# Kernel tuning notes

Measured on AMD Instinct MI355X. Metric: run time of the kernel, lower is better.

## Reference

```python
import jax, jax.numpy as jnp
import numpy as np

EPS = 1e-12      # F.normalize eps
LN_EPS = 1e-5    # nn.LayerNorm eps
SLOPE = 0.01     # LeakyReLU negative slope
SCALE = 5.0      # attention temperature used by the module


def _l2norm(x):
    n = jnp.sqrt(jnp.sum(x * x, axis=-1, keepdims=True))
    return x / jnp.maximum(n, EPS)


def _layer_norm(x, g, b):
    m = jnp.mean(x, axis=-1, keepdims=True)
    v = jnp.mean((x - m) ** 2, axis=-1, keepdims=True)
    return (x - m) / jnp.sqrt(v + LN_EPS) * g + b


def _leaky(x):
    return jnp.where(x >= 0, x, SLOPE * x)


def setup_inputs() -> dict:
    key = jax.random.key(0)
    ks = jax.random.split(key, 18)
    B, T, N, C = 8, 8, 25, 256
    n = T * N  # 200 == num_nodes
    inp = {
        "local_feat": jax.random.normal(ks[0], (B, T, N, C), dtype=jnp.float32),
        "global_feat": jax.random.normal(ks[1], (B, C), dtype=jnp.float32),
        "pos": jax.random.uniform(ks[2], (B, T, N, 9), dtype=jnp.float32),
        # Diff_prop params
        "dp_adj_w": jax.random.normal(ks[3], (C, C), dtype=jnp.float32) / np.sqrt(C),
        "dp_aff_w": jax.random.normal(ks[4], (C, C), dtype=jnp.float32) * np.sqrt(2.0 / C),
        "dp_aff_b": jnp.zeros((C,), dtype=jnp.float32),
        "dp_ln_g": jnp.ones((C,), dtype=jnp.float32),
        "dp_ln_b": jnp.zeros((C,), dtype=jnp.float32),
        # Feat_aggr params
        "fa_adj_w": jax.random.normal(ks[5], (C, C), dtype=jnp.float32) / np.sqrt(C),
        "fa_aff_w": jax.random.normal(ks[6], (C, C), dtype=jnp.float32) * np.sqrt(2.0 / C),
        "fa_aff_b": jnp.zeros((C,), dtype=jnp.float32),
        "fa_ln_g": jnp.ones((C,), dtype=jnp.float32),
        "fa_ln_b": jnp.zeros((C,), dtype=jnp.float32),
        # Node_att params (Linear(num_nodes+9, 1): weight [1, n+9])
        "na_w": jax.random.normal(ks[7], (1, n + 9), dtype=jnp.float32) * np.sqrt(2.0 / (n + 9)),
        "na_b": jnp.zeros((1,), dtype=jnp.float32),
    }
    return inp


def _diff_prop(lf4, adj_w, aff_w, aff_b, ln_g, ln_b):
    B, T, N, C = lf4.shape
    n = T * N
    lf = lf4.reshape(B, n, C)
    nf = _l2norm(lf)
    # quadratic-form attention: A[b,i,j] = nf_i W nf_j
    A = jnp.einsum('bnc,cd,bmd->bnm', nf, adj_w, nf)
    A = jnp.exp(SCALE * (A - jnp.max(A, axis=-1, keepdims=True)))
    A = A * (1.0 - jnp.eye(n, dtype=A.dtype))
    A = A / jnp.maximum(jnp.sum(A, axis=-1, keepdims=True), EPS)  # L1 row norm (A>=0)
    # full pairwise difference tensor [B, n, n, C]
    diff = lf[:, :, None, :] - lf[:, None, :, :]
    diff = jnp.einsum('bijc,dc->bijd', diff, aff_w) + aff_b
    agg = jnp.einsum('bij,bijd->bid', A, diff)
    out = _leaky(_layer_norm(agg, ln_g, ln_b))
    return out.reshape(B, T, N, C)


def _feat_aggr(lf4, adj_w, aff_w, aff_b, ln_g, ln_b):
    B, T, N, C = lf4.shape
    n = T * N
    lf = lf4.reshape(B, n, C)
    nf = _l2norm(lf)
    A = jnp.einsum('bnc,cd,bmd->bnm', nf, adj_w, nf)
    A = jax.nn.softmax(SCALE * (A - jnp.max(A, axis=-1, keepdims=True)), axis=-1)
    lf = jnp.einsum('bnc,dc->bnd', lf, aff_w) + aff_b
    lf = jnp.einsum('bij,bjk->bik', A, lf)
    out = _leaky(_layer_norm(lf, ln_g, ln_b))
    return out.reshape(B, T, N, C)


def _node_att(lf4, pos, w, b):
    B, T, N, C = lf4.shape
    n = T * N
    lf = lf4.reshape(B, n, C)
    p = pos.reshape(B, n, -1)
    nf = _l2norm(lf)
    A = jnp.einsum('bnc,bmc->bnm', nf, nf)            # [B, n, n]
    src = jnp.concatenate([A, p], axis=-1)            # [B, n, n+9]
    att = jax.nn.sigmoid(jnp.einsum('bni,oi->bno', src, w) + b)  # [B, n, 1]
    att = att.reshape(B, T, N, 1)
    return lf4 * att


def reference(local_feat, global_feat, pos,
              dp_adj_w, dp_aff_w, dp_aff_b, dp_ln_g, dp_ln_b,
              fa_adj_w, fa_aff_w, fa_aff_b, fa_ln_g, fa_ln_b,
              na_w, na_b):
    x = _diff_prop(local_feat, dp_adj_w, dp_aff_w, dp_aff_b, dp_ln_g, dp_ln_b)
    x = _feat_aggr(x, fa_adj_w, fa_aff_w, fa_aff_b, fa_ln_g, fa_ln_b)
    x = _node_att(x, pos, na_w, na_b)
    return x
```

## Files before the change

### kernel.cpp

```cpp
#include <hip/hip_runtime.h>
#include <math.h>

#define Bn 8
#define NN 200
#define Cc 256
#define RR (Bn*NN)
#define JP 200
#define N_EPS 1e-12f
#define LN_EPS 1e-5f
#define SLOPE 0.01f
#define SCALE 5.0f

#define FMA4(acc, s, v) { acc.x = fmaf((s), (v).x, acc.x); acc.y = fmaf((s), (v).y, acc.y); \
                          acc.z = fmaf((s), (v).z, acc.z); acc.w = fmaf((s), (v).w, acc.w); }

__device__ __forceinline__ float wave_reduce_sum(float v) {
    #pragma unroll
    for (int o = 32; o > 0; o >>= 1) v += __shfl_xor(v, o);
    return v;
}

__device__ __forceinline__ float2 half_reduce_sum2(float2 v, float* sh, int h) {
    __syncthreads();
    #pragma unroll
    for (int o = 32; o > 0; o >>= 1) { v.x += __shfl_xor(v.x, o); v.y += __shfl_xor(v.y, o); }
    int w = threadIdx.x >> 6;
    if ((threadIdx.x & 63) == 0) { sh[w*2] = v.x; sh[w*2+1] = v.y; }
    __syncthreads();
    int b0 = h * 8;
    return make_float2(sh[b0]+sh[b0+2]+sh[b0+4]+sh[b0+6],
                       sh[b0+1]+sh[b0+3]+sh[b0+5]+sh[b0+7]);
}

__device__ __forceinline__ float2 half_reduce_max2(float2 v, float* sh, int h) {
    __syncthreads();
    #pragma unroll
    for (int o = 32; o > 0; o >>= 1) {
        v.x = fmaxf(v.x, __shfl_xor(v.x, o));
        v.y = fmaxf(v.y, __shfl_xor(v.y, o));
    }
    int w = threadIdx.x >> 6;
    if ((threadIdx.x & 63) == 0) { sh[w*2] = v.x; sh[w*2+1] = v.y; }
    __syncthreads();
    int b0 = h * 8;
    return make_float2(fmaxf(fmaxf(sh[b0],sh[b0+2]), fmaxf(sh[b0+4],sh[b0+6])),
                       fmaxf(fmaxf(sh[b0+1],sh[b0+3]), fmaxf(sh[b0+5],sh[b0+7])));
}

__global__ void k_pre(const float* __restrict__ lf, const float* __restrict__ dp_adj_w,
                      const float* __restrict__ dp_aff_w, const float* __restrict__ fa_aff_w,
                      float* __restrict__ nfT, float* __restrict__ M,
                      float* __restrict__ WT1, float* __restrict__ WT2) {
    __shared__ __align__(16) float sx[8][Cc];
    __shared__ __align__(16) float buf[8192];
    __shared__ float tile[32][33];
    int bid = blockIdx.x;
    int t = threadIdx.x, lane = t & 63, wvi = t >> 6;
    if (bid < RR/8) {
        int r0 = bid * 8;
        #pragma unroll
        for (int k = 0; k < 2; k++) {
            int r = 2*wvi + k;
            float4 x = ((const float4*)(lf + (size_t)(r0 + r) * Cc))[lane];
            float ss = wave_reduce_sum(x.x*x.x + x.y*x.y + x.z*x.z + x.w*x.w);
            float inv = 1.f / fmaxf(sqrtf(ss), N_EPS);
            x.x *= inv; x.y *= inv; x.z *= inv; x.w *= inv;
            ((float4*)&sx[r][0])[lane] = x;
        }
        __syncthreads();
        {
            int b = r0 / NN, i0 = r0 % NN;
            float4 cA, cB;
            cA.x = sx[0][t]; cA.y = sx[1][t]; cA.z = sx[2][t]; cA.w = sx[3][t];
            cB.x = sx[4][t]; cB.y = sx[5][t]; cB.z = sx[6][t]; cB.w = sx[7][t];
            float* np = nfT + (size_t)b * Cc * JP + (size_t)t * JP + i0;
            *((float4*)np) = cA;
            *((float4*)(np + 4)) = cB;
        }
        int qc = t & 63, cid = t >> 6;
        int c0 = cid * 64;
        float4 z = make_float4(0.f,0.f,0.f,0.f);
        float4 acc0=z, acc1=z, acc2=z, acc3=z, acc4=z, acc5=z, acc6=z, acc7=z;
        #pragma unroll 4
        for (int c4 = c0; c4 < c0 + 64; c4 += 4) {
            float4 w0 = *(const float4*)(dp_adj_w + (size_t)(c4+0) * Cc + 4*qc);
            float4 w1 = *(const float4*)(dp_adj_w + (size_t)(c4+1) * Cc + 4*qc);
            float4 w2 = *(const float4*)(dp_adj_w + (size_t)(c4+2) * Cc + 4*qc);
            float4 w3 = *(const float4*)(dp_adj_w + (size_t)(c4+3) * Cc + 4*qc);
            float4 xr;
            xr = *(const float4*)(&sx[0][c4]);
            FMA4(acc0, xr.x, w0); FMA4(acc0, xr.y, w1); FMA4(acc0, xr.z, w2); FMA4(acc0, xr.w, w3);
            xr = *(const float4*)(&sx[1][c4]);
            FMA4(acc1, xr.x, w0); FMA4(acc1, xr.y, w1); FMA4(acc1, xr.z, w2); FMA4(acc1, xr.w, w3);
            xr = *(const float4*)(&sx[2][c4]);
            FMA4(acc2, xr.x, w0); FMA4(acc2, xr.y, w1); FMA4(acc2, xr.z, w2); FMA4(acc2, xr.w, w3);
            xr = *(const float4*)(&sx[3][c4]);
            FMA4(acc3, xr.x, w0); FMA4(acc3, xr.y, w1); FMA4(acc3, xr.z, w2); FMA4(acc3, xr.w, w3);
            xr = *(const float4*)(&sx[4][c4]);
            FMA4(acc4, xr.x, w0); FMA4(acc4, xr.y, w1); FMA4(acc4, xr.z, w2); FMA4(acc4, xr.w, w3);
            xr = *(const float4*)(&sx[5][c4]);
            FMA4(acc5, xr.x, w0); FMA4(acc5, xr.y, w1); FMA4(acc5, xr.z, w2); FMA4(acc5, xr.w, w3);
            xr = *(const float4*)(&sx[6][c4]);
            FMA4(acc6, xr.x, w0); FMA4(acc6, xr.y, w1); FMA4(acc6, xr.z, w2); FMA4(acc6, xr.w, w3);
            xr = *(const float4*)(&sx[7][c4]);
            FMA4(acc7, xr.x, w0); FMA4(acc7, xr.y, w1); FMA4(acc7, xr.z, w2); FMA4(acc7, xr.w, w3);
        }
        float4* b4 = (float4*)buf;
        int o = cid * 512 + qc;
        b4[o      ] = acc0; b4[o +  64] = acc1; b4[o + 128] = acc2; b4[o + 192] = acc3;
        b4[o + 256] = acc4; b4[o + 320] = acc5; b4[o + 384] = acc6; b4[o + 448] = acc7;
        __syncthreads();
        #pragma unroll
        for (int k = 0; k < 2; k++) {
            int o4 = t + k*256;
            int r = o4 >> 6, qc2 = o4 & 63;
            float4 s0 = b4[o4], s1 = b4[512 + o4], s2 = b4[1024 + o4], s3 = b4[1536 + o4];
            float4 sv;
            sv.x = (s0.x + s1.x) + (s2.x + s3.x);
            sv.y = (s0.y + s1.y) + (s2.y + s3.y);
            sv.z = (s0.z + s1.z) + (s2.z + s3.z);
            sv.w = (s0.w + s1.w) + (s2.w + s3.w);
            *(float4*)(M + (size_t)(r0 + r) * Cc + 4*qc2) = sv;
        }
    } else {
        int tb = bid - RR/8;
        const float* S; float* D;
        if (tb < 64) { S = dp_aff_w; D = WT1; } else { S = fa_aff_w; D = WT2; tb -= 64; }
        int bx = tb & 7, by = tb >> 3;
        int tx = t & 31, ty = t >> 5;
        #pragma unroll
        for (int k = 0; k < 32; k += 8)
            tile[ty + k][tx] = S[(size_t)(by*32 + ty + k) * Cc + bx*32 + tx];
        __syncthreads();
        #pragma unroll
        for (int k = 0; k < 32; k += 8)
            D[(size_t)(bx*32 + ty + k) * Cc + by*32 + tx] = tile[tx][ty + k];
    }
}

__global__ void k_row1f(const float* __restrict__ nfT, const float* __restrict__ Min,
                        const float* __restrict__ lf, const float* __restrict__ dp_aff_b,
                        const float* __restrict__ WT1,
                        const float* __restrict__ g, const float* __restrict__ bb,
                        const float* __restrict__ fa_adj_w, const float* __restrict__ WT2,
                        const float* __restrict__ fa_aff_b,
                        float* __restrict__ nfT2, float* __restrict__ M2,
                        float* __restrict__ lf2) {
    __shared__ __align__(16) float smT[Cc*4];
    __shared__ __align__(16) float saraw[4*NN];
    __shared__ __align__(16) float saT[NN*4];
    __shared__ __align__(16) float suT[Cc*4];
    __shared__ __align__(16) float buf[8192];
    __shared__ float sh[16];
    __shared__ float sinv[4];
    int t = threadIdx.x, h = t >> 8, tt = t & 255;
    int b = blockIdx.x & 7;
    int i0 = (blockIdx.x >> 3) * 4;
    size_t base = (size_t)b * NN * Cc;
    {
        const float* src = Min + base + (size_t)i0 * Cc;
        #pragma unroll
        for (int o = t; o < 1024; o += 512) {
            int c = o >> 2, r = o & 3;
            smT[o] = src[(size_t)r * Cc + c];
        }
    }
    __syncthreads();
    {
        int q = t & 63, cid = t >> 6;
        if (q < 50) {
            int c0 = cid * 32;
            const float* nfp = nfT + (size_t)b * Cc * JP + (size_t)c0 * JP + 4*q;
            float4 z4 = make_float4(0.f,0.f,0.f,0.f);
            float4 a0 = z4, a1 = z4, a2 = z4, a3 = z4;
            #pragma unroll 8
            for (int c = 0; c < 32; c++) {
                float4 v  = *(const float4*)(nfp + (size_t)c * JP);
                float4 mv = *(const float4*)(&smT[(c0 + c) * 4]);
                FMA4(a0, mv.x, v); FMA4(a1, mv.y, v);
                FMA4(a2, mv.z, v); FMA4(a3, mv.w, v);
            }
            float* pp = buf + cid * 800 + 4*q;
            *(float4*)(pp      ) = a0;
            *(float4*)(pp + 200) = a1;
            *(float4*)(pp + 400) = a2;
            *(float4*)(pp + 600) = a3;
        }
    }
    __syncthreads();
    for (int o = t; o < 800; o += 512) {
        float s = 0.f;
        #pragma unroll
        for (int p = 0; p < 8; p++) s += buf[p*800 + o];
        saraw[o] = s;
    }
    __syncthreads();
    int lr0 = h, lr1 = h + 2;
    float2 vm;
    vm.x = (tt < NN) ? saraw[lr0*NN + tt] : -INFINITY;
    vm.y = (tt < NN) ? saraw[lr1*NN + tt] : -INFINITY;
    float2 m = half_reduce_max2(vm, sh, h);
    float e0 = (tt < NN && tt != i0 + lr0) ? expf(SCALE * (vm.x - m.x)) : 0.f;
    float e1 = (tt < NN && tt != i0 + lr1) ? expf(SCALE * (vm.y - m.y)) : 0.f;
    float2 sum = half_reduce_sum2(make_float2(e0, e1), sh, h);
    if (tt < NN) {
        saT[tt*4 + lr0] = e0 / fmaxf(sum.x, N_EPS);
        saT[tt*4 + lr1] = e1 / fmaxf(sum.y, N_EPS);
    }
    float s0 = sum.x / fmaxf(sum.x, N_EPS);
    float s1 = sum.y / fmaxf(sum.y, N_EPS);
    __syncthreads();
    const float* lfb = lf + base;
    {
        int qc = t & 63, jc = t >> 6;
        int j0 = jc * 25;
        float4 z4 = make_float4(0.f,0.f,0.f,0.f);
        float4 u0 = z4, u1 = z4, u2 = z4, u3 = z4;
        #pragma unroll 5
        for (int j = j0; j < j0 + 25; j++) {
            float4 pv = *(const float4*)(lfb + (size_t)j * Cc + 4*qc);
            float4 av = *(const float4*)(&saT[j*4]);
            FMA4(u0, av.x, pv); FMA4(u1, av.y, pv);
            FMA4(u2, av.z, pv); FMA4(u3, av.w, pv);
        }
        float* pp = buf + jc*1024 + 4*qc;
        *(float4*)(pp      ) = u0;
        *(float4*)(pp + 256) = u1;
        *(float4*)(pp + 512) = u2;
        *(float4*)(pp + 768) = u3;
    }
    __syncthreads();
    float acc0 = 0.f, acc1 = 0.f;
    #pragma unroll
    for (int p = 0; p < 8; p++) { acc0 += buf[p*1024 + t]; acc1 += buf[p*1024 + t + 512]; }
    float U0 = fmaf(s0, lfb[(size_t)(i0 + lr0) * Cc + tt], -acc0);
    float U1 = fmaf(s1, lfb[(size_t)(i0 + lr1) * Cc + tt], -acc1);
    __syncthreads();
    smT[tt*4 + lr0] = U0;
    smT[tt*4 + lr1] = U1;
    __syncthreads();
    {
        int qc = t & 63, cid = t >> 6;
        int c0 = cid * 32;
        float4 z4 = make_float4(0.f,0.f,0.f,0.f);
        float4 p0 = z4, p1 = z4, p2 = z4, p3 = z4;
        #pragma unroll 8
        for (int c = c0; c < c0 + 32; c++) {
            float4 wv = *(const float4*)(WT1 + (size_t)c * Cc + 4*qc);
            float4 uv = *(const float4*)(&smT[c*4]);
            FMA4(p0, uv.x, wv); FMA4(p1, uv.y, wv);
            FMA4(p2, uv.z, wv); FMA4(p3, uv.w, wv);
        }
        float* pp = buf + cid*1024 + 4*qc;
        *(float4*)(pp      ) = p0;
        *(float4*)(pp + 256) = p1;
        *(float4*)(pp + 512) = p2;
        *(float4*)(pp + 768) = p3;
    }
    __syncthreads();
    float y0 = 0.f, y1 = 0.f;
    #pragma unroll
    for (int p = 0; p < 8; p++) { y0 += buf[p*1024 + t]; y1 += buf[p*1024 + t + 512]; }
    float bv = dp_aff_b[tt];
    y0 += s0 * bv;
    y1 += s1 * bv;
    float gg = g[tt], bbv = bb[tt];
    float2 mean2 = half_reduce_sum2(make_float2(y0, y1), sh, h);
    float d0 = y0 - mean2.x * (1.f/256.f);
    float d1 = y1 - mean2.y * (1.f/256.f);
    float2 var2 = half_reduce_sum2(make_float2(d0*d0, d1*d1), sh, h);
    float z0 = d0 / sqrtf(var2.x * (1.f/256.f) + LN_EPS) * gg + bbv;
    float z1 = d1 / sqrtf(var2.y * (1.f/256.f) + LN_EPS) * gg + bbv;
    z0 = (z0 >= 0.f) ? z0 : SLOPE * z0;
    z1 = (z1 >= 0.f) ? z1 : SLOPE * z1;
    suT[tt*4 + lr0] = z0; suT[tt*4 + lr1] = z1;
    float2 ss2 = half_reduce_sum2(make_float2(z0*z0, z1*z1), sh, h);
    if (tt == 0) {
        sinv[lr0] = 1.f / fmaxf(sqrtf(ss2.x), N_EPS);
        sinv[lr1] = 1.f / fmaxf(sqrtf(ss2.y), N_EPS);
    }
    __syncthreads();
    if (h == 0) {
        float4 col;
        col.x = suT[tt*4+0] * sinv[0]; col.y = suT[tt*4+1] * sinv[1];
        col.z = suT[tt*4+2] * sinv[2]; col.w = suT[tt*4+3] * sinv[3];
        *((float4*)(nfT2 + (size_t)b * Cc * JP + (size_t)tt * JP + i0)) = col;
    }
    {
        int qc = t & 63, gidx = t >> 6;
        int mt = gidx & 1, cch = gidx >> 1;
        const float* Wm = mt ? WT2 : fa_adj_w;
        int c0 = cch * 64;
        float4 z4 = make_float4(0.f,0.f,0.f,0.f);
        float4 d0v = z4, d1v = z4, d2v = z4, d3v = z4;
        #pragma unroll 8
        for (int c = c0; c < c0 + 64; c++) {
            float4 wv = *(const float4*)(Wm + (size_t)c * Cc + 4*qc);
            float4 uv = *(const float4*)(&suT[c*4]);
            FMA4(d0v, uv.x, wv); FMA4(d1v, uv.y, wv);
            FMA4(d2v, uv.z, wv); FMA4(d3v, uv.w, wv);
        }
        float* pp = buf + cch*2048 + mt*1024 + 4*qc;
        *(float4*)(pp      ) = d0v;
        *(float4*)(pp + 256) = d1v;
        *(float4*)(pp + 512) = d2v;
        *(float4*)(pp + 768) = d3v;
    }
    __syncthreads();
    {
        float4* b4 = (float4*)buf;
        int o4 = t;
        int mt2 = o4 >> 8, r2 = (o4 >> 6) & 3, qc2 = o4 & 63;
        float4 v0 = b4[o4], v1 = b4[512 + o4], v2 = b4[1024 + o4], v3 = b4[1536 + o4];
        float4 sv;
        sv.x = (v0.x + v1.x) + (v2.x + v3.x);
        sv.y = (v0.y + v1.y) + (v2.y + v3.y);
        sv.z = (v0.z + v1.z) + (v2.z + v3.z);
        sv.w = (v0.w + v1.w) + (v2.w + v3.w);
        if (mt2 == 0) {
            float sc = sinv[r2];
            sv.x *= sc; sv.y *= sc; sv.z *= sc; sv.w *= sc;
            *(float4*)(M2 + base + (size_t)(i0 + r2) * Cc + 4*qc2) = sv;
        } else {
            float4 fb = *(const float4*)(fa_aff_b + 4*qc2);
            sv.x += fb.x; sv.y += fb.y; sv.z += fb.z; sv.w += fb.w;
            *(float4*)(lf2 + base + (size_t)(i0 + r2) * Cc + 4*qc2) = sv;
        }
    }
}

__global__ void k_row2f(const float* __restrict__ nfT2, const float* __restrict__ M2,
                        const float* __restrict__ lf2, const float* __restrict__ g,
                        const float* __restrict__ bb, float* __restrict__ x2,
                        float* __restrict__ nf3) {
    __shared__ __align__(16) float smT[Cc*4];
    __shared__ __align__(16) float saraw[4*NN];
    __shared__ __align__(16) float saT[NN*4];
    __shared__ __align__(16) float buf[8192];
    __shared__ float sh[16];
    int t = threadIdx.x, h = t >> 8, tt = t & 255;
    int b = blockIdx.x & 7;
    int i0 = (blockIdx.x >> 3) * 4;
    size_t base = (size_t)b * NN * Cc;
    {
        const float* src = M2 + base + (size_t)i0 * Cc;
        #pragma unroll
        for (int o = t; o < 1024; o += 512) {
            int c = o >> 2, r = o & 3;
            smT[o] = src[(size_t)r * Cc + c];
        }
    }
    __syncthreads();
    {
        int q = t & 63, cid = t >> 6;
        if (q < 50) {
            int c0 = cid * 32;
            const float* nfp = nfT2 + (size_t)b * Cc * JP + (size_t)c0 * JP + 4*q;
            float4 z4 = make_float4(0.f,0.f,0.f,0.f);
            float4 a0 = z4, a1 = z4, a2 = z4, a3 = z4;
            #pragma unroll 8
            for (int c = 0; c < 32; c++) {
                float4 v  = *(const float4*)(nfp + (size_t)c * JP);
                float4 mv = *(const float4*)(&smT[(c0 + c) * 4]);
                FMA4(a0, mv.x, v); FMA4(a1, mv.y, v);
                FMA4(a2, mv.z, v); FMA4(a3, mv.w, v);
            }
            float* pp = buf + cid * 800 + 4*q;
            *(float4*)(pp      ) = a0;
            *(float4*)(pp + 200) = a1;
            *(float4*)(pp + 400) = a2;
            *(float4*)(pp + 600) = a3;
        }
    }
    __syncthreads();
    for (int o = t; o < 800; o += 512) {
        float s = 0.f;
        #pragma unroll
        for (int p = 0; p < 8; p++) s += buf[p*800 + o];
        saraw[o] = s;
    }
    __syncthreads();
    int lr0 = h, lr1 = h + 2;
    float2 vm;
    vm.x = (tt < NN) ? saraw[lr0*NN + tt] : -INFINITY;
    vm.y = (tt < NN) ? saraw[lr1*NN + tt] : -INFINITY;
    float2 m = half_reduce_max2(vm, sh, h);
    float e0 = (tt < NN) ? expf(SCALE * (vm.x - m.x)) : 0.f;
    float e1 = (tt < NN) ? expf(SCALE * (vm.y - m.y)) : 0.f;
    float2 sum = half_reduce_sum2(make_float2(e0, e1), sh, h);
    if (tt < NN) { saT[tt*4 + lr0] = e0 / sum.x; saT[tt*4 + lr1] = e1 / sum.y; }
    __syncthreads();
    const float* l2b = lf2 + base;
    {
        int qc = t & 63, jc = t >> 6;
        int j0 = jc * 25;
        float4 z4 = make_float4(0.f,0.f,0.f,0.f);
        float4 u0 = z4, u1 = z4, u2 = z4, u3 = z4;
        #pragma unroll 5
        for (int j = j0; j < j0 + 25; j++) {
            float4 pv = *(const float4*)(l2b + (size_t)j * Cc + 4*qc);
            float4 av = *(const float4*)(&saT[j*4]);
            FMA4(u0, av.x, pv); FMA4(u1, av.y, pv);
            FMA4(u2, av.z, pv); FMA4(u3, av.w, pv);
        }
        float* pp = buf + jc*1024 + 4*qc;
        *(float4*)(pp      ) = u0;
        *(float4*)(pp + 256) = u1;
        *(float4*)(pp + 512) = u2;
        *(float4*)(pp + 768) = u3;
    }
    __syncthreads();
    float y0 = 0.f, y1 = 0.f;
    #pragma unroll
    for (int p = 0; p < 8; p++) { y0 += buf[p*1024 + t]; y1 += buf[p*1024 + t + 512]; }
    float gg = g[tt], bbv = bb[tt];
    float2 mean2 = half_reduce_sum2(make_float2(y0, y1), sh, h);
    float d0 = y0 - mean2.x * (1.f/256.f);
    float d1 = y1 - mean2.y * (1.f/256.f);
    float2 var2 = half_reduce_sum2(make_float2(d0*d0, d1*d1), sh, h);
    float z0 = d0 / sqrtf(var2.x * (1.f/256.f) + LN_EPS) * gg + bbv;
    float z1 = d1 / sqrtf(var2.y * (1.f/256.f) + LN_EPS) * gg + bbv;
    z0 = (z0 >= 0.f) ? z0 : SLOPE * z0;
    z1 = (z1 >= 0.f) ? z1 : SLOPE * z1;
    x2[base + (size_t)(i0 + lr0) * Cc + tt] = z0;
    x2[base + (size_t)(i0 + lr1) * Cc + tt] = z1;
    float2 ss2 = half_reduce_sum2(make_float2(z0*z0, z1*z1), sh, h);
    nf3[base + (size_t)(i0 + lr0) * Cc + tt] = z0 / fmaxf(sqrtf(ss2.x), N_EPS);
    nf3[base + (size_t)(i0 + lr1) * Cc + tt] = z1 / fmaxf(sqrtf(ss2.y), N_EPS);
}

__global__ void k_natt(const float* __restrict__ x2, const float* __restrict__ nf3,
                       const float* __restrict__ pos, const float* __restrict__ w,
                       const float* __restrict__ nb, float* __restrict__ out) {
    __shared__ float svb[4][Cc];
    int t = threadIdx.x, lane = t & 63, wv = t >> 6;
    int b = blockIdx.x & 7;
    int i = (blockIdx.x >> 3) * 4 + wv;
    const float4* slab = (const float4*)(nf3 + (size_t)b * NN * Cc);
    float4 acc = make_float4(0.f, 0.f, 0.f, 0.f);
    for (int j = wv * 50; j < wv * 50 + 50; j++) {
        float4 q = slab[j * 64 + lane];
        float wj = w[j];
        acc.x = fmaf(wj, q.x, acc.x);
        acc.y = fmaf(wj, q.y, acc.y);
        acc.z = fmaf(wj, q.z, acc.z);
        acc.w = fmaf(wj, q.w, acc.w);
    }
    ((float4*)&svb[wv][0])[lane] = acc;
    __syncthreads();
    float4 p0 = ((const float4*)&svb[0][0])[lane];
    float4 p1 = ((const float4*)&svb[1][0])[lane];
    float4 p2 = ((const float4*)&svb[2][0])[lane];
    float4 p3 = ((const float4*)&svb[3][0])[lane];
    float4 vb;
    vb.x = (p0.x + p1.x) + (p2.x + p3.x);
    vb.y = (p0.y + p1.y) + (p2.y + p3.y);
    vb.z = (p0.z + p1.z) + (p2.z + p3.z);
    vb.w = (p0.w + p1.w) + (p2.w + p3.w);
    size_t bi = (size_t)b * NN + i;
    float4 nv = ((const float4*)(nf3 + bi * Cc))[lane];
    float val = nv.x*vb.x + nv.y*vb.y + nv.z*vb.z + nv.w*vb.w;
    if (lane < 9) val += pos[bi * 9 + lane] * w[NN + lane];
    val = wave_reduce_sum(val);
    float att = 1.f / (1.f + expf(-(val + nb[0])));
    float4 xo = ((const float4*)(x2 + bi * Cc))[lane];
    xo.x *= att; xo.y *= att; xo.z *= att; xo.w *= att;
    ((float4*)(out + bi * Cc))[lane] = xo;
}

extern "C" void kernel_launch(void* const* d_in, const int* in_sizes, int n_in,
                              void* d_out, int out_size, void* d_ws, size_t ws_size,
                              hipStream_t stream) {
    (void)in_sizes; (void)n_in; (void)out_size; (void)ws_size;
    const float* lf       = (const float*)d_in[0];
    const float* pos      = (const float*)d_in[2];
    const float* dp_adj_w = (const float*)d_in[3];
    const float* dp_aff_w = (const float*)d_in[4];
    const float* dp_aff_b = (const float*)d_in[5];
    const float* dp_ln_g  = (const float*)d_in[6];
    const float* dp_ln_b  = (const float*)d_in[7];
    const float* fa_adj_w = (const float*)d_in[8];
    const float* fa_aff_w = (const float*)d_in[9];
    const float* fa_aff_b = (const float*)d_in[10];
    const float* fa_ln_g  = (const float*)d_in[11];
    const float* fa_ln_b  = (const float*)d_in[12];
    const float* na_w     = (const float*)d_in[13];
    const float* na_b     = (const float*)d_in[14];
    float* out = (float*)d_out;
    float* ws  = (float*)d_ws;

    float* nfT  = ws;
    float* nfT2 = nfT  + Bn * Cc * JP;
    float* M    = nfT2 + Bn * Cc * JP;
    float* lf2  = M    + RR * Cc;
    float* x2   = lf2  + RR * Cc;
    float* nf3  = x2   + RR * Cc;
    float* WT1  = nf3  + RR * Cc;
    float* WT2  = WT1  + Cc * Cc;

    k_pre  <<<RR/8 + 128, dim3(256), 0, stream>>>(lf, dp_adj_w, dp_aff_w, fa_aff_w,
                                                  nfT, M, WT1, WT2);
    k_row1f<<<Bn * NN/4,  dim3(512), 0, stream>>>(nfT, M, lf, dp_aff_b, WT1,
                                                  dp_ln_g, dp_ln_b, fa_adj_w, WT2, fa_aff_b,
                                                  nfT2, M, lf2);
    k_row2f<<<Bn * NN/4,  dim3(512), 0, stream>>>(nfT2, M, lf2, fa_ln_g, fa_ln_b, x2, nf3);
    k_natt <<<Bn * NN/4,  dim3(256), 0, stream>>>(x2, nf3, pos, na_w, na_b, out);
}
```

Before: 61.73 us.

## Process eight rows per block in k_row1f to reuse weight loads

k_row1f now handles 8 query rows per block instead of 4, halving the grid. The weight GEMM phases (WT1, fa_adj_w, WT2) each load a weight float4 once and apply it to 8 rows, halving global weight traffic per row. In exchange the block count drops to 200, which reduces parallelism on a large GPU. Shared memory use and per-thread register pressure also grow, and the attention phases run twice serially.

```diff
diff --git a/kernel.cpp b/kernel.cpp
--- a/kernel.cpp
+++ b/kernel.cpp
@@ -146,186 +146,226 @@
                         const float* __restrict__ fa_aff_b,
                         float* __restrict__ nfT2, float* __restrict__ M2,
                         float* __restrict__ lf2) {
-    __shared__ __align__(16) float smT[Cc*4];
-    __shared__ __align__(16) float saraw[4*NN];
-    __shared__ __align__(16) float saT[NN*4];
-    __shared__ __align__(16) float suT[Cc*4];
+    __shared__ __align__(16) float smT[Cc*8];
+    __shared__ __align__(16) float saraw[8*NN];
+    __shared__ __align__(16) float saT[NN*8];
+    __shared__ __align__(16) float suT[Cc*8];
     __shared__ __align__(16) float buf[8192];
     __shared__ float sh[16];
-    __shared__ float sinv[4];
+    __shared__ float sinv[8];
     int t = threadIdx.x, h = t >> 8, tt = t & 255;
     int b = blockIdx.x & 7;
-    int i0 = (blockIdx.x >> 3) * 4;
+    int i0 = (blockIdx.x >> 3) * 8;
     size_t base = (size_t)b * NN * Cc;
     {
         const float* src = Min + base + (size_t)i0 * Cc;
         #pragma unroll
-        for (int o = t; o < 1024; o += 512) {
-            int c = o >> 2, r = o & 3;
+        for (int o = t; o < 2048; o += 512) {
+            int c = o >> 3, r = o & 7;
             smT[o] = src[(size_t)r * Cc + c];
         }
     }
     __syncthreads();
-    {
-        int q = t & 63, cid = t >> 6;
-        if (q < 50) {
-            int c0 = cid * 32;
-            const float* nfp = nfT + (size_t)b * Cc * JP + (size_t)c0 * JP + 4*q;
+    #pragma unroll
+    for (int p = 0; p < 2; p++) {
+        {
+            int q = t & 63, cid = t >> 6;
+            if (q < 50) {
+                int c0 = cid * 32;
+                const float* nfp = nfT + (size_t)b * Cc * JP + (size_t)c0 * JP + 4*q;
+                float4 z4 = make_float4(0.f,0.f,0.f,0.f);
+                float4 a0 = z4, a1 = z4, a2 = z4, a3 = z4;
+                #pragma unroll 8
+                for (int c = 0; c < 32; c++) {
+                    float4 v  = *(const float4*)(nfp + (size_t)c * JP);
+                    float4 mv = *(const float4*)(&smT[(c0 + c) * 8 + 4*p]);
+                    FMA4(a0, mv.x, v); FMA4(a1, mv.y, v);
+                    FMA4(a2, mv.z, v); FMA4(a3, mv.w, v);
+                }
+                float* pp = buf + cid * 800 + 4*q;
+                *(float4*)(pp      ) = a0;
+                *(float4*)(pp + 200) = a1;
+                *(float4*)(pp + 400) = a2;
+                *(float4*)(pp + 600) = a3;
+            }
+        }
+        __syncthreads();
+        for (int o = t; o < 800; o += 512) {
+            float s = 0.f;
+            #pragma unroll
+            for (int q8 = 0; q8 < 8; q8++) s += buf[q8*800 + o];
+            saraw[p*800 + o] = s;
+        }
+        __syncthreads();
+    }
+    float sv[4];
+    #pragma unroll
+    for (int k = 0; k < 2; k++) {
+        int rA = 4*k + h, rB = 4*k + h + 2;
+        float2 vm;
+        vm.x = (tt < NN) ? saraw[rA*NN + tt] : -INFINITY;
+        vm.y = (tt < NN) ? saraw[rB*NN + tt] : -INFINITY;
+        float2 m = half_reduce_max2(vm, sh, h);
+        float e0 = (tt < NN && tt != i0 + rA) ? expf(SCALE * (vm.x - m.x)) : 0.f;
+        float e1 = (tt < NN && tt != i0 + rB) ? expf(SCALE * (vm.y - m.y)) : 0.f;
+        float2 sum = half_reduce_sum2(make_float2(e0, e1), sh, h);
+        if (tt < NN) {
+            saT[tt*8 + rA] = e0 / fmaxf(sum.x, N_EPS);
+            saT[tt*8 + rB] = e1 / fmaxf(sum.y, N_EPS);
+        }
+        sv[2*k]   = sum.x / fmaxf(sum.x, N_EPS);
+        sv[2*k+1] = sum.y / fmaxf(sum.y, N_EPS);
+    }
+    __syncthreads();
+    const float* lfb = lf + base;
+    #pragma unroll
+    for (int p = 0; p < 2; p++) {
+        {
+            int qc = t & 63, jc = t >> 6;
+            int j0 = jc * 25;
             float4 z4 = make_float4(0.f,0.f,0.f,0.f);
-            float4 a0 = z4, a1 = z4, a2 = z4, a3 = z4;
-            #pragma unroll 8
-            for (int c = 0; c < 32; c++) {
-                float4 v  = *(const float4*)(nfp + (size_t)c * JP);
-                float4 mv = *(const float4*)(&smT[(c0 + c) * 4]);
-                FMA4(a0, mv.x, v); FMA4(a1, mv.y, v);
-                FMA4(a2, mv.z, v); FMA4(a3, mv.w, v);
+            float4 u0 = z4, u1 = z4, u2 = z4, u3 = z4;
+            #pragma unroll 5
+            for (int j = j0; j < j0 + 25; j++) {
+                float4 pv = *(const float4*)(lfb + (size_t)j * Cc + 4*qc);
+                float4 av = *(const float4*)(&saT[j*8 + 4*p]);
+                FMA4(u0, av.x, pv); FMA4(u1, av.y, pv);
+                FMA4(u2, av.z, pv); FMA4(u3, av.w, pv);
             }
-            float* pp = buf + cid * 800 + 4*q;
-            *(float4*)(pp      ) = a0;
-            *(float4*)(pp + 200) = a1;
-            *(float4*)(pp + 400) = a2;
-            *(float4*)(pp + 600) = a3;
-        }
-    }
-    __syncthreads();
-    for (int o = t; o < 800; o += 512) {
-        float s = 0.f;
-        #pragma unroll
-        for (int p = 0; p < 8; p++) s += buf[p*800 + o];
-        saraw[o] = s;
-    }
-    __syncthreads();
-    int lr0 = h, lr1 = h + 2;
-    float2 vm;
-    vm.x = (tt < NN) ? saraw[lr0*NN + tt] : -INFINITY;
-    vm.y = (tt < NN) ? saraw[lr1*NN + tt] : -INFINITY;
-    float2 m = half_reduce_max2(vm, sh, h);
-    float e0 = (tt < NN && tt != i0 + lr0) ? expf(SCALE * (vm.x - m.x)) : 0.f;
-    float e1 = (tt < NN && tt != i0 + lr1) ? expf(SCALE * (vm.y - m.y)) : 0.f;
-    float2 sum = half_reduce_sum2(make_float2(e0, e1), sh, h);
-    if (tt < NN) {
-        saT[tt*4 + lr0] = e0 / fmaxf(sum.x, N_EPS);
-        saT[tt*4 + lr1] = e1 / fmaxf(sum.y, N_EPS);
-    }
-    float s0 = sum.x / fmaxf(sum.x, N_EPS);
-    float s1 = sum.y / fmaxf(sum.y, N_EPS);
-    __syncthreads();
-    const float* lfb = lf + base;
-    {
-        int qc = t & 63, jc = t >> 6;
-        int j0 = jc * 25;
-        float4 z4 = make_float4(0.f,0.f,0.f,0.f);
-        float4 u0 = z4, u1 = z4, u2 = z4, u3 = z4;
-        #pragma unroll 5
-        for (int j = j0; j < j0 + 25; j++) {
-            float4 pv = *(const float4*)(lfb + (size_t)j * Cc + 4*qc);
-            float4 av = *(const float4*)(&saT[j*4]);
-            FMA4(u0, av.x, pv); FMA4(u1, av.y, pv);
-            FMA4(u2, av.z, pv); FMA4(u3, av.w, pv);
-        }
-        float* pp = buf + jc*1024 + 4*qc;
-        *(float4*)(pp      ) = u0;
-        *(float4*)(pp + 256) = u1;
-        *(float4*)(pp + 512) = u2;
-        *(float4*)(pp + 768) = u3;
-    }
-    __syncthreads();
-    float acc0 = 0.f, acc1 = 0.f;
-    #pragma unroll
-    for (int p = 0; p < 8; p++) { acc0 += buf[p*1024 + t]; acc1 += buf[p*1024 + t + 512]; }
-    float U0 = fmaf(s0, lfb[(size_t)(i0 + lr0) * Cc + tt], -acc0);
-    float U1 = fmaf(s1, lfb[(size_t)(i0 + lr1) * Cc + tt], -acc1);
-    __syncthreads();
-    smT[tt*4 + lr0] = U0;
-    smT[tt*4 + lr1] = U1;
-    __syncthreads();
+            float* pp = buf + jc*1024 + 4*qc;
+            *(float4*)(pp      ) = u0;
+            *(float4*)(pp + 256) = u1;
+            *(float4*)(pp + 512) = u2;
+            *(float4*)(pp + 768) = u3;
+        }
+        __syncthreads();
+        float acc0 = 0.f, acc1 = 0.f;
+        #pragma unroll
+        for (int q8 = 0; q8 < 8; q8++) { acc0 += buf[q8*1024 + t]; acc1 += buf[q8*1024 + t + 512]; }
+        int rA = 4*p + h, rB = 4*p + h + 2;
+        float U0 = fmaf(sv[2*p],   lfb[(size_t)(i0 + rA) * Cc + tt], -acc0);
+        float U1 = fmaf(sv[2*p+1], lfb[(size_t)(i0 + rB) * Cc + tt], -acc1);
+        smT[tt*8 + rA] = U0;
+        smT[tt*8 + rB] = U1;
+        __syncthreads();
+    }
     {
         int qc = t & 63, cid = t >> 6;
-        int c0 = cid * 32;
-        float4 z4 = make_float4(0.f,0.f,0.f,0.f);
-        float4 p0 = z4, p1 = z4, p2 = z4, p3 = z4;
-        #pragma unroll 8
-        for (int c = c0; c < c0 + 32; c++) {
-            float4 wv = *(const float4*)(WT1 + (size_t)c * Cc + 4*qc);
-            float4 uv = *(const float4*)(&smT[c*4]);
-            FMA4(p0, uv.x, wv); FMA4(p1, uv.y, wv);
-            FMA4(p2, uv.z, wv); FMA4(p3, uv.w, wv);
-        }
-        float* pp = buf + cid*1024 + 4*qc;
-        *(float4*)(pp      ) = p0;
-        *(float4*)(pp + 256) = p1;
-        *(float4*)(pp + 512) = p2;
-        *(float4*)(pp + 768) = p3;
-    }
-    __syncthreads();
-    float y0 = 0.f, y1 = 0.f;
-    #pragma unroll
-    for (int p = 0; p < 8; p++) { y0 += buf[p*1024 + t]; y1 += buf[p*1024 + t + 512]; }
-    float bv = dp_aff_b[tt];
-    y0 += s0 * bv;
-    y1 += s1 * bv;
+        if (cid < 4) {
+            int c0 = cid * 64;
+            float4 z4 = make_float4(0.f,0.f,0.f,0.f);
+            float4 pA0=z4,pA1=z4,pA2=z4,pA3=z4,pB0=z4,pB1=z4,pB2=z4,pB3=z4;
+            #pragma unroll 4
+            for (int c = c0; c < c0 + 64; c++) {
+                float4 wv = *(const float4*)(WT1 + (size_t)c * Cc + 4*qc);
+                float4 uA = *(const float4*)(&smT[c*8]);
+                float4 uB = *(const float4*)(&smT[c*8 + 4]);
+                FMA4(pA0, uA.x, wv); FMA4(pA1, uA.y, wv);
+                FMA4(pA2, uA.z, wv); FMA4(pA3, uA.w, wv);
+                FMA4(pB0, uB.x, wv); FMA4(pB1, uB.y, wv);
+                FMA4(pB2, uB.z, wv); FMA4(pB3, uB.w, wv);
+            }
+            float* pp = buf + cid*2048 + 4*qc;
+            *(float4*)(pp       ) = pA0; *(float4*)(pp +  256) = pA1;
+            *(float4*)(pp +  512) = pA2; *(float4*)(pp +  768) = pA3;
+            *(float4*)(pp + 1024) = pB0; *(float4*)(pp + 1280) = pB1;
+            *(float4*)(pp + 1536) = pB2; *(float4*)(pp + 1792) = pB3;
+        }
+    }
+    __syncthreads();
+    float y0, y1, y2, y3;
+    {
+        float bv = dp_aff_b[tt];
+        int rA = h, rB = h + 2, rC = 4 + h, rD = 6 + h;
+        y0 = sv[0]*bv; y1 = sv[1]*bv; y2 = sv[2]*bv; y3 = sv[3]*bv;
+        #pragma unroll
+        for (int q8 = 0; q8 < 4; q8++) {
+            y0 += buf[q8*2048 + rA*256 + tt];
+            y1 += buf[q8*2048 + rB*256 + tt];
+            y2 += buf[q8*2048 + rC*256 + tt];
+            y3 += buf[q8*2048 + rD*256 + tt];
+        }
+    }
     float gg = g[tt], bbv = bb[tt];
-    float2 mean2 = half_reduce_sum2(make_float2(y0, y1), sh, h);
-    float d0 = y0 - mean2.x * (1.f/256.f);
-    float d1 = y1 - mean2.y * (1.f/256.f);
-    float2 var2 = half_reduce_sum2(make_float2(d0*d0, d1*d1), sh, h);
-    float z0 = d0 / sqrtf(var2.x * (1.f/256.f) + LN_EPS) * gg + bbv;
-    float z1 = d1 / sqrtf(var2.y * (1.f/256.f) + LN_EPS) * gg + bbv;
-    z0 = (z0 >= 0.f) ? z0 : SLOPE * z0;
-    z1 = (z1 >= 0.f) ? z1 : SLOPE * z1;
-    suT[tt*4 + lr0] = z0; suT[tt*4 + lr1] = z1;
-    float2 ss2 = half_reduce_sum2(make_float2(z0*z0, z1*z1), sh, h);
-    if (tt == 0) {
-        sinv[lr0] = 1.f / fmaxf(sqrtf(ss2.x), N_EPS);
-        sinv[lr1] = 1.f / fmaxf(sqrtf(ss2.y), N_EPS);
+    #pragma unroll
+    for (int k = 0; k < 2; k++) {
+        float ya = (k == 0) ? y0 : y2;
+        float yb = (k == 0) ? y1 : y3;
+        int rA = 4*k + h, rB = 4*k + h + 2;
+        float2 mean2 = half_reduce_sum2(make_float2(ya, yb), sh, h);
+        float d0 = ya - mean2.x * (1.f/256.f);
+        float d1 = yb - mean2.y * (1.f/256.f);
+        float2 var2 = half_reduce_sum2(make_float2(d0*d0, d1*d1), sh, h);
+        float z0 = d0 / sqrtf(var2.x * (1.f/256.f) + LN_EPS) * gg + bbv;
+        float z1 = d1 / sqrtf(var2.y * (1.f/256.f) + LN_EPS) * gg + bbv;
+        z0 = (z0 >= 0.f) ? z0 : SLOPE * z0;
+        z1 = (z1 >= 0.f) ? z1 : SLOPE * z1;
+        suT[tt*8 + rA] = z0;
+        suT[tt*8 + rB] = z1;
+        float2 ss2 = half_reduce_sum2(make_float2(z0*z0, z1*z1), sh, h);
+        if (tt == 0) {
+            sinv[rA] = 1.f / fmaxf(sqrtf(ss2.x), N_EPS);
+            sinv[rB] = 1.f / fmaxf(sqrtf(ss2.y), N_EPS);
+        }
     }
     __syncthreads();
     if (h == 0) {
-        float4 col;
-        col.x = suT[tt*4+0] * sinv[0]; col.y = suT[tt*4+1] * sinv[1];
-        col.z = suT[tt*4+2] * sinv[2]; col.w = suT[tt*4+3] * sinv[3];
-        *((float4*)(nfT2 + (size_t)b * Cc * JP + (size_t)tt * JP + i0)) = col;
-    }
-    {
-        int qc = t & 63, gidx = t >> 6;
-        int mt = gidx & 1, cch = gidx >> 1;
+        float4 cA, cB;
+        cA.x = suT[tt*8+0]*sinv[0]; cA.y = suT[tt*8+1]*sinv[1];
+        cA.z = suT[tt*8+2]*sinv[2]; cA.w = suT[tt*8+3]*sinv[3];
+        cB.x = suT[tt*8+4]*sinv[4]; cB.y = suT[tt*8+5]*sinv[5];
+        cB.z = suT[tt*8+6]*sinv[6]; cB.w = suT[tt*8+7]*sinv[7];
+        float* np = nfT2 + (size_t)b * Cc * JP + (size_t)tt * JP + i0;
+        *((float4*)np) = cA;
+        *((float4*)(np + 4)) = cB;
+    }
+    #pragma unroll
+    for (int mt = 0; mt < 2; mt++) {
         const float* Wm = mt ? WT2 : fa_adj_w;
-        int c0 = cch * 64;
-        float4 z4 = make_float4(0.f,0.f,0.f,0.f);
-        float4 d0v = z4, d1v = z4, d2v = z4, d3v = z4;
-        #pragma unroll 8
-        for (int c = c0; c < c0 + 64; c++) {
-            float4 wv = *(const float4*)(Wm + (size_t)c * Cc + 4*qc);
-            float4 uv = *(const float4*)(&suT[c*4]);
-            FMA4(d0v, uv.x, wv); FMA4(d1v, uv.y, wv);
-            FMA4(d2v, uv.z, wv); FMA4(d3v, uv.w, wv);
-        }
-        float* pp = buf + cch*2048 + mt*1024 + 4*qc;
-        *(float4*)(pp      ) = d0v;
-        *(float4*)(pp + 256) = d1v;
-        *(float4*)(pp + 512) = d2v;
-        *(float4*)(pp + 768) = d3v;
-    }
-    __syncthreads();
-    {
-        float4* b4 = (float4*)buf;
-        int o4 = t;
-        int mt2 = o4 >> 8, r2 = (o4 >> 6) & 3, qc2 = o4 & 63;
-        float4 v0 = b4[o4], v1 = b4[512 + o4], v2 = b4[1024 + o4], v3 = b4[1536 + o4];
-        float4 sv;
-        sv.x = (v0.x + v1.x) + (v2.x + v3.x);
-        sv.y = (v0.y + v1.y) + (v2.y + v3.y);
-        sv.z = (v0.z + v1.z) + (v2.z + v3.z);
-        sv.w = (v0.w + v1.w) + (v2.w + v3.w);
-        if (mt2 == 0) {
-            float sc = sinv[r2];
-            sv.x *= sc; sv.y *= sc; sv.z *= sc; sv.w *= sc;
-            *(float4*)(M2 + base + (size_t)(i0 + r2) * Cc + 4*qc2) = sv;
-        } else {
-            float4 fb = *(const float4*)(fa_aff_b + 4*qc2);
-            sv.x += fb.x; sv.y += fb.y; sv.z += fb.z; sv.w += fb.w;
-            *(float4*)(lf2 + base + (size_t)(i0 + r2) * Cc + 4*qc2) = sv;
-        }
+        {
+            int qc = t & 63, cid = t >> 6;
+            if (cid < 4) {
+                int c0 = cid * 64;
+                float4 z4 = make_float4(0.f,0.f,0.f,0.f);
+                float4 pA0=z4,pA1=z4,pA2=z4,pA3=z4,pB0=z4,pB1=z4,pB2=z4,pB3=z4;
+                #pragma unroll 4
+                for (int c = c0; c < c0 + 64; c++) {
+                    float4 wv = *(const float4*)(Wm + (size_t)c * Cc + 4*qc);
+                    float4 uA = *(const float4*)(&suT[c*8]);
+                    float4 uB = *(const float4*)(&suT[c*8 + 4]);
+                    FMA4(pA0, uA.x, wv); FMA4(pA1, uA.y, wv);
+                    FMA4(pA2, uA.z, wv); FMA4(pA3, uA.w, wv);
+                    FMA4(pB0, uB.x, wv); FMA4(pB1, uB.y, wv);
+                    FMA4(pB2, uB.z, wv); FMA4(pB3, uB.w, wv);
+                }
+                float* pp = buf + cid*2048 + 4*qc;
+                *(float4*)(pp       ) = pA0; *(float4*)(pp +  256) = pA1;
+                *(float4*)(pp +  512) = pA2; *(float4*)(pp +  768) = pA3;
+                *(float4*)(pp + 1024) = pB0; *(float4*)(pp + 1280) = pB1;
+                *(float4*)(pp + 1536) = pB2; *(float4*)(pp + 1792) = pB3;
+            }
+        }
+        __syncthreads();
+        {
+            float4* b4 = (float4*)buf;
+            int r = t >> 6, qc2 = t & 63;
+            float4 v0 = b4[t], v1 = b4[512 + t], v2 = b4[1024 + t], v3 = b4[1536 + t];
+            float4 svv;
+            svv.x = (v0.x + v1.x) + (v2.x + v3.x);
+            svv.y = (v0.y + v1.y) + (v2.y + v3.y);
+            svv.z = (v0.z + v1.z) + (v2.z + v3.z);
+            svv.w = (v0.w + v1.w) + (v2.w + v3.w);
+            if (mt == 0) {
+                float sc = sinv[r];
+                svv.x *= sc; svv.y *= sc; svv.z *= sc; svv.w *= sc;
+                *(float4*)(M2 + base + (size_t)(i0 + r) * Cc + 4*qc2) = svv;
+            } else {
+                float4 fb = *(const float4*)(fa_aff_b + 4*qc2);
+                svv.x += fb.x; svv.y += fb.y; svv.z += fb.z; svv.w += fb.w;
+                *(float4*)(lf2 + base + (size_t)(i0 + r) * Cc + 4*qc2) = svv;
+            }
+        }
+        __syncthreads();
     }
 }
 
@@ -500,7 +540,7 @@
 
     k_pre  <<<RR/8 + 128, dim3(256), 0, stream>>>(lf, dp_adj_w, dp_aff_w, fa_aff_w,
                                                   nfT, M, WT1, WT2);
-    k_row1f<<<Bn * NN/4,  dim3(512), 0, stream>>>(nfT, M, lf, dp_aff_b, WT1,
+    k_row1f<<<Bn * NN/8,  dim3(512), 0, stream>>>(nfT, M, lf, dp_aff_b, WT1,
                                                   dp_ln_g, dp_ln_b, fa_adj_w, WT2, fa_aff_b,
                                                   nfT2, M, lf2);
     k_row2f<<<Bn * NN/4,  dim3(512), 0, stream>>>(nfT2, M, lf2, fa_ln_g, fa_ln_b, x2, nf3);
```

Measured after the change: 72.30 us. 17.1% more time.
